# Optimization experiments

Measured on AMD Instinct MI355X. Metric: run time of the kernel, lower is better.

Reference implementation:

```python
import jax, jax.numpy as jnp
import numpy as np

TEMPERATURE = 34.0
PAD = 1  # kernel_size // 2

def setup_inputs() -> dict:
    key = jax.random.key(0)
    ks = jax.random.split(key, 5)
    B, C, H, W = 32, 256, 56, 56
    K, O, I, kh = 4, 256, 256, 3
    hidden = int(C * 0.25) + 1  # 65
    return {
        "x": jax.random.normal(ks[0], (B, C, H, W), jnp.float32),
        "fc1_w": jax.random.normal(ks[1], (hidden, C), jnp.float32) * (2.0 / C) ** 0.5,
        "fc2_w": jax.random.normal(ks[2], (K, hidden), jnp.float32) * (2.0 / hidden) ** 0.5,
        "fc2_b": jnp.zeros((K,), jnp.float32),
        "weight": jax.random.normal(ks[3], (K, O, I, kh, kh), jnp.float32) * (2.0 / (I * kh * kh)) ** 0.5,
        "bias": jnp.zeros((K, O), jnp.float32),
    }

def reference(x, fc1_w, fc2_w, fc2_b, weight, bias):
    # attention2d: global avg pool -> 1x1 conv (fc1) -> relu -> 1x1 conv (fc2) -> softmax(logits/T)
    pooled = x.mean(axis=(2, 3))                      # [B, C]
    h = jax.nn.relu(pooled @ fc1_w.T)                 # [B, hidden]
    logits = h @ fc2_w.T + fc2_b                      # [B, K]
    att = jax.nn.softmax(logits / TEMPERATURE, axis=1)
    # aggregate per-sample conv weights/bias over K kernel banks
    agg_w = jnp.einsum('bk,koihw->boihw', att, weight)  # [B, O, I, kh, kw]
    agg_b = att @ bias                                  # [B, O]
    # per-sample conv (torch emulates via groups=B): vmap over batch
    def conv_one(xi, wi):
        return jax.lax.conv_general_dilated(
            xi[None], wi, window_strides=(1, 1),
            padding=((PAD, PAD), (PAD, PAD)),
            dimension_numbers=('NCHW', 'OIHW', 'NCHW'))[0]
    out = jax.vmap(conv_one)(x, agg_w)                 # [B, O, H, W]
    return out + agg_b[:, :, None, None]
```

## Files before the change

### kernel.cpp

```cpp
#include <hip/hip_runtime.h>


typedef short bf16x8 __attribute__((ext_vector_type(8)));
typedef float f32x16 __attribute__((ext_vector_type(16)));

__device__ __forceinline__ unsigned short f2bf(float f) {
  unsigned int u = __float_as_uint(f);
  return (unsigned short)((u + 0x7FFFu + ((u >> 16) & 1u)) >> 16);
}
__device__ __forceinline__ float bf2f(unsigned short h) {
  return __uint_as_float(((unsigned int)h) << 16);
}

__device__ __forceinline__ int invswz(int S) {
  int b7 = (S >> 7) & 1;
  int b6 = ((S >> 6) & 1) ^ b7;
  int b5 = ((S >> 5) & 1) ^ b6;
  int b4 = ((S >> 4) & 1) ^ b5;
  return (S & ~0x70) | (b4 << 4) | (b5 << 5) | (b6 << 6);
}

typedef const __attribute__((address_space(1))) unsigned int* gas_t;
typedef __attribute__((address_space(3))) unsigned int* las_t;
__device__ __forceinline__ void dma16(const void* g, unsigned lds_addr) {
  __builtin_amdgcn_global_load_lds((gas_t)g, (las_t)(size_t)lds_addr, 16, 0, 0);
}

__global__ void xcast_k(const float* __restrict__ x, unsigned short* __restrict__ xb,
                        float* __restrict__ pooled) {
  __shared__ unsigned short tile[64 * 260];
  int b = blockIdx.y;
  int hw0 = blockIdx.x * 64;
  int t = threadIdx.x;
  int p = t & 15, g = t >> 4;
#pragma unroll
  for (int i = 0; i < 16; ++i) {
    int c = g + 16 * i;
    float4 v = *(const float4*)(x + ((size_t)(b * 256 + c)) * 3136 + hw0 + p * 4);
    tile[(p * 4 + 0) * 260 + c] = f2bf(v.x);
    tile[(p * 4 + 1) * 260 + c] = f2bf(v.y);
    tile[(p * 4 + 2) * 260 + c] = f2bf(v.z);
    tile[(p * 4 + 3) * 260 + c] = f2bf(v.w);
  }
  __syncthreads();
  int lane = t & 63, wq = t >> 6;
  int c4 = lane * 4;
#pragma unroll
  for (int it = 0; it < 16; ++it) {
    int hl = it * 4 + wq;
    ushort4 v = *(const ushort4*)&tile[hl * 260 + c4];
    *(ushort4*)&xb[((size_t)(b * 3136 + hw0 + hl)) * 256 + c4] = v;
  }
  float s = 0.f;
#pragma unroll 16
  for (int hl = 0; hl < 64; ++hl) s += bf2f(tile[hl * 260 + t]);
  atomicAdd(&pooled[b * 256 + t], s * (1.0f / 3136.0f));
}

__global__ void att_k(const float* __restrict__ pooled, const float* __restrict__ fc1,
                      const float* __restrict__ fc2w, const float* __restrict__ fc2b,
                      const float* __restrict__ bias, float* __restrict__ att,
                      float* __restrict__ aggb) {
  int b = blockIdx.x, t = threadIdx.x;
  __shared__ float p[256];
  __shared__ float h[65];
  __shared__ float a4[4];
  for (int i = t; i < 256; i += 64) p[i] = pooled[b * 256 + i];
  __syncthreads();
  for (int j = t; j < 65; j += 64) {
    float s = 0.f;
    for (int c = 0; c < 256; ++c) s += p[c] * fc1[j * 256 + c];
    h[j] = fmaxf(s, 0.f);
  }
  __syncthreads();
  if (t == 0) {
    float lg[4];
    for (int k = 0; k < 4; ++k) {
      float s = fc2b[k];
      for (int j = 0; j < 65; ++j) s += h[j] * fc2w[k * 65 + j];
      lg[k] = s * (1.0f / 34.0f);
    }
    float m = fmaxf(fmaxf(lg[0], lg[1]), fmaxf(lg[2], lg[3]));
    float e0 = expf(lg[0] - m), e1 = expf(lg[1] - m), e2 = expf(lg[2] - m), e3 = expf(lg[3] - m);
    float inv = 1.0f / (e0 + e1 + e2 + e3);
    a4[0] = e0 * inv; a4[1] = e1 * inv; a4[2] = e2 * inv; a4[3] = e3 * inv;
    for (int k = 0; k < 4; ++k) att[b * 4 + k] = a4[k];
  }
  __syncthreads();
  for (int o = t; o < 256; o += 64) {
    float s = 0.f;
    for (int k = 0; k < 4; ++k) s += a4[k] * bias[k * 256 + o];
    aggb[b * 256 + o] = s;
  }
}

__global__ void aggw_k(const float* __restrict__ weight, const float* __restrict__ att,
                       unsigned short* __restrict__ aggw) {
  __shared__ float wl[4 * 2304];
  int o = blockIdx.x, t = threadIdx.x;
  for (int k = 0; k < 4; ++k)
    for (int idx = t; idx < 2304; idx += 256)
      wl[k * 2304 + idx] = weight[((size_t)(k * 256 + o)) * 2304 + idx];
  __syncthreads();
  int ot = o >> 7, ol = o & 127, ic = t >> 4, il = t & 15;
  int b0 = blockIdx.y * 8;
  for (int b = b0; b < b0 + 8; ++b) {
    float a0 = att[b * 4 + 0], a1 = att[b * 4 + 1], a2 = att[b * 4 + 2], a3 = att[b * 4 + 3];
    size_t base = ((size_t)((b * 2 + ot) * 16 + ic)) * (9 * 2048) + ol * 16 + il;
#pragma unroll
    for (int r = 0; r < 9; ++r) {
      float s = a0 * wl[t * 9 + r] + a1 * wl[2304 + t * 9 + r] +
                a2 * wl[4608 + t * 9 + r] + a3 * wl[6912 + t * 9 + r];
      aggw[base + r * 2048] = f2bf(s);
    }
  }
}

#define XBUF 16384
#define AOFF 32768

__global__ __launch_bounds__(256, 2) void conv_k(const unsigned short* __restrict__ xb,
                                                 const unsigned short* __restrict__ aggw,
                                                 const float* __restrict__ aggb,
                                                 const float* __restrict__ zerobuf,
                                                 float* __restrict__ out) {
  extern __shared__ unsigned char lds[];
  const unsigned ldsbase = (unsigned)(size_t)&lds[0];
  const int t = threadIdx.x;
  const int wid = t >> 6, lane = t & 63, l31 = lane & 31, q = lane >> 5;
  const int wo = wid >> 1, wn = wid & 1;

  int id = blockIdx.x;
  int wgid = (id & 7) * 104 + (id >> 3);
  int bn = wgid % 13;
  int rest = wgid / 13;
  int b = rest >> 1, bo = rest & 1;

  const int o0 = bo * 128;
  const int n0 = bn * 256;
  const int h0 = n0 / 56;

  int bbase[4], nn[4], swz[4][3];
#pragma unroll
  for (int nf = 0; nf < 4; ++nf) {
    int n = n0 + wn * 128 + nf * 32 + l31;
    int h = n / 56, w = n - h * 56;
    nn[nf] = n;
    bbase[nf] = ((h - h0) * 64 + w) * 32 + q * 16;
#pragma unroll
    for (int dw = 0; dw < 3; ++dw) swz[nf][dw] = ((w + dw) & 7) << 4;
  }
  int abase[2];
#pragma unroll
  for (int mf = 0; mf < 2; ++mf) {
    int ol = wo * 64 + mf * 32 + l31;
    abase[mf] = AOFF + ((ol * 32 + q * 16) ^ ((ol & 7) << 4));
  }

  const char* xb_b = (const char*)xb + (size_t)b * 3136 * 512;
  const char* ag_c = (const char*)aggw + (size_t)rest * 589824;

  const char* xg[4];
#pragma unroll
  for (int j = 0; j < 4; ++j) {
    int S = (j * 256 + t) * 16;
    int L = invswz(S);
    int pos = L >> 5, sub = (L >> 4) & 1;
    int row = pos >> 6, col = pos & 63;
    int hg = h0 - 1 + row, wg = col - 1;
    bool valid = (col >= 1 && col <= 56 && hg >= 0 && hg < 56);
    xg[j] = valid ? (xb_b + (size_t)(hg * 56 + wg) * 512 + sub * 16) : (const char*)zerobuf;
  }
  const char* aL = ag_c + invswz(t * 16);

  f32x16 acc[2][4];
#pragma unroll
  for (int i = 0; i < 2; ++i)
#pragma unroll
    for (int j = 0; j < 4; ++j)
#pragma unroll
      for (int e = 0; e < 16; ++e) acc[i][j][e] = 0.f;

#pragma unroll
  for (int j = 0; j < 4; ++j) dma16(xg[j], ldsbase + j * 4096 + wid * 1024);
#pragma unroll
  for (int j = 0; j < 9; ++j) dma16(aL + j * 4096, ldsbase + AOFF + j * 4096 + wid * 1024);
  __syncthreads();

  int cur = 0;
  for (int ic = 0; ic < 16; ++ic) {
    const unsigned char* xlds = lds + cur * XBUF;
#pragma unroll
    for (int r = 0; r < 9; ++r) {
      const int dh = r / 3, dw = r % 3;
      bf16x8 a0 = *(const bf16x8*)(lds + abase[0] + r * 4096);
      bf16x8 a1 = *(const bf16x8*)(lds + abase[1] + r * 4096);
      bf16x8 b0 = *(const bf16x8*)(xlds + ((bbase[0] + dh * 2048 + dw * 32) ^ swz[0][dw]));
      bf16x8 b1 = *(const bf16x8*)(xlds + ((bbase[1] + dh * 2048 + dw * 32) ^ swz[1][dw]));
      bf16x8 b2 = *(const bf16x8*)(xlds + ((bbase[2] + dh * 2048 + dw * 32) ^ swz[2][dw]));
      bf16x8 b3 = *(const bf16x8*)(xlds + ((bbase[3] + dh * 2048 + dw * 32) ^ swz[3][dw]));
      __builtin_amdgcn_s_setprio(1);
      acc[0][0] = __builtin_amdgcn_mfma_f32_32x32x16_bf16(a0, b0, acc[0][0], 0, 0, 0);
      acc[0][1] = __builtin_amdgcn_mfma_f32_32x32x16_bf16(a0, b1, acc[0][1], 0, 0, 0);
      acc[0][2] = __builtin_amdgcn_mfma_f32_32x32x16_bf16(a0, b2, acc[0][2], 0, 0, 0);
      acc[0][3] = __builtin_amdgcn_mfma_f32_32x32x16_bf16(a0, b3, acc[0][3], 0, 0, 0);
      acc[1][0] = __builtin_amdgcn_mfma_f32_32x32x16_bf16(a1, b0, acc[1][0], 0, 0, 0);
      acc[1][1] = __builtin_amdgcn_mfma_f32_32x32x16_bf16(a1, b1, acc[1][1], 0, 0, 0);
      acc[1][2] = __builtin_amdgcn_mfma_f32_32x32x16_bf16(a1, b2, acc[1][2], 0, 0, 0);
      acc[1][3] = __builtin_amdgcn_mfma_f32_32x32x16_bf16(a1, b3, acc[1][3], 0, 0, 0);
      __builtin_amdgcn_s_setprio(0);
      if (r == 0 && ic + 1 < 16) {
#pragma unroll
        for (int j = 0; j < 4; ++j)
          dma16(xg[j] + (ic + 1) * 32, ldsbase + (cur ^ 1) * XBUF + j * 4096 + wid * 1024);
      }
    }
    __syncthreads();
    if (ic + 1 < 16) {
#pragma unroll
      for (int j = 0; j < 9; ++j)
        dma16(aL + (size_t)(ic + 1) * 36864 + j * 4096, ldsbase + AOFF + j * 4096 + wid * 1024);
      __syncthreads();
    }
    cur ^= 1;
  }

#pragma unroll
  for (int mf = 0; mf < 2; ++mf) {
#pragma unroll
    for (int reg = 0; reg < 16; ++reg) {
      int o = o0 + wo * 64 + mf * 32 + (reg & 3) + 8 * (reg >> 2) + 4 * q;
      float ab = aggb[b * 256 + o];
      float* op = out + ((size_t)(b * 256 + o)) * 3136;
#pragma unroll
      for (int nf = 0; nf < 4; ++nf) {
        if (nn[nf] < 3136) op[nn[nf]] = acc[mf][nf][reg] + ab;
      }
    }
  }
}

extern "C" void kernel_launch(void* const* d_in, const int* in_sizes, int n_in,
                              void* d_out, int out_size, void* d_ws, size_t ws_size,
                              hipStream_t stream) {
  const float* x      = (const float*)d_in[0];
  const float* fc1    = (const float*)d_in[1];
  const float* fc2w   = (const float*)d_in[2];
  const float* fc2b   = (const float*)d_in[3];
  const float* weight = (const float*)d_in[4];
  const float* bias   = (const float*)d_in[5];
  float* out = (float*)d_out;

  char* ws = (char*)d_ws;
  float* pooled         = (float*)(ws);
  float* att            = (float*)(ws + 32768);
  float* aggb           = (float*)(ws + 33280);
  unsigned short* aggw  = (unsigned short*)(ws + 66048);
  unsigned short* xb    = (unsigned short*)(ws + 66048 + 37748736);

  hipFuncSetAttribute(reinterpret_cast<const void*>(conv_k),
                      hipFuncAttributeMaxDynamicSharedMemorySize, 2 * XBUF + 36864);

  hipMemsetAsync(pooled, 0, 32768, stream);
  xcast_k<<<dim3(49, 32), 256, 0, stream>>>(x, xb, pooled);
  att_k<<<32, 64, 0, stream>>>(pooled, fc1, fc2w, fc2b, bias, att, aggb);
  hipMemsetAsync(pooled, 0, 1024, stream);
  aggw_k<<<dim3(256, 4), 256, 0, stream>>>(weight, att, aggw);
  conv_k<<<832, 256, 2 * XBUF + 36864, stream>>>(xb, aggw, aggb, (const float*)pooled, out);
}
```

Measured before the change: 232.7 us.

## Load aggregated weights directly into registers instead of staging through LDS

The conv kernel no longer stages per-sample weight tiles in LDS. Each wave now loads its A fragments for all nine taps straight from global memory into registers at the start of every channel chunk, and the x-tile prefetch moves to the same point. This drops the second barrier and cuts shared memory from about 69KB to 32KB per block, which may let more blocks fit per CU. The costs are higher register pressure (18 extra bf16x8 values per thread) and exposed global-load latency on the weight reads, since those are not double-buffered.

Result: slower. 257.1 us (+10.5%).

```diff
diff --git a/kernel.cpp b/kernel.cpp
--- a/kernel.cpp
+++ b/kernel.cpp
@@ -117,14 +117,13 @@
 }
 
 #define XBUF 16384
-#define AOFF 32768
 
 __global__ __launch_bounds__(256, 2) void conv_k(const unsigned short* __restrict__ xb,
                                                  const unsigned short* __restrict__ aggw,
                                                  const float* __restrict__ aggb,
                                                  const float* __restrict__ zerobuf,
                                                  float* __restrict__ out) {
-  extern __shared__ unsigned char lds[];
+  __shared__ __align__(16) unsigned char lds[2 * XBUF];
   const unsigned ldsbase = (unsigned)(size_t)&lds[0];
   const int t = threadIdx.x;
   const int wid = t >> 6, lane = t & 63, l31 = lane & 31, q = lane >> 5;
@@ -150,12 +149,9 @@
 #pragma unroll
     for (int dw = 0; dw < 3; ++dw) swz[nf][dw] = ((w + dw) & 7) << 4;
   }
-  int abase[2];
-#pragma unroll
-  for (int mf = 0; mf < 2; ++mf) {
-    int ol = wo * 64 + mf * 32 + l31;
-    abase[mf] = AOFF + ((ol * 32 + q * 16) ^ ((ol & 7) << 4));
-  }
+  int aoff[2];
+#pragma unroll
+  for (int mf = 0; mf < 2; ++mf) aoff[mf] = (wo * 64 + mf * 32 + l31) * 32 + q * 16;
 
   const char* xb_b = (const char*)xb + (size_t)b * 3136 * 512;
   const char* ag_c = (const char*)aggw + (size_t)rest * 589824;
@@ -171,7 +167,6 @@
     bool valid = (col >= 1 && col <= 56 && hg >= 0 && hg < 56);
     xg[j] = valid ? (xb_b + (size_t)(hg * 56 + wg) * 512 + sub * 16) : (const char*)zerobuf;
   }
-  const char* aL = ag_c + invswz(t * 16);
 
   f32x16 acc[2][4];
 #pragma unroll
@@ -183,45 +178,43 @@
 
 #pragma unroll
   for (int j = 0; j < 4; ++j) dma16(xg[j], ldsbase + j * 4096 + wid * 1024);
-#pragma unroll
-  for (int j = 0; j < 9; ++j) dma16(aL + j * 4096, ldsbase + AOFF + j * 4096 + wid * 1024);
   __syncthreads();
 
   int cur = 0;
   for (int ic = 0; ic < 16; ++ic) {
+    bf16x8 areg[2][9];
+    const char* agc = ag_c + (size_t)ic * 36864;
+#pragma unroll
+    for (int r = 0; r < 9; ++r) {
+      areg[0][r] = *(const bf16x8*)(agc + r * 4096 + aoff[0]);
+      areg[1][r] = *(const bf16x8*)(agc + r * 4096 + aoff[1]);
+    }
+    if (ic + 1 < 16) {
+#pragma unroll
+      for (int j = 0; j < 4; ++j)
+        dma16(xg[j] + (ic + 1) * 32, ldsbase + (cur ^ 1) * XBUF + j * 4096 + wid * 1024);
+    }
+    __builtin_amdgcn_sched_barrier(0);
     const unsigned char* xlds = lds + cur * XBUF;
 #pragma unroll
     for (int r = 0; r < 9; ++r) {
       const int dh = r / 3, dw = r % 3;
-      bf16x8 a0 = *(const bf16x8*)(lds + abase[0] + r * 4096);
-      bf16x8 a1 = *(const bf16x8*)(lds + abase[1] + r * 4096);
       bf16x8 b0 = *(const bf16x8*)(xlds + ((bbase[0] + dh * 2048 + dw * 32) ^ swz[0][dw]));
       bf16x8 b1 = *(const bf16x8*)(xlds + ((bbase[1] + dh * 2048 + dw * 32) ^ swz[1][dw]));
       bf16x8 b2 = *(const bf16x8*)(xlds + ((bbase[2] + dh * 2048 + dw * 32) ^ swz[2][dw]));
       bf16x8 b3 = *(const bf16x8*)(xlds + ((bbase[3] + dh * 2048 + dw * 32) ^ swz[3][dw]));
       __builtin_amdgcn_s_setprio(1);
-      acc[0][0] = __builtin_amdgcn_mfma_f32_32x32x16_bf16(a0, b0, acc[0][0], 0, 0, 0);
-      acc[0][1] = __builtin_amdgcn_mfma_f32_32x32x16_bf16(a0, b1, acc[0][1], 0, 0, 0);
-      acc[0][2] = __builtin_amdgcn_mfma_f32_32x32x16_bf16(a0, b2, acc[0][2], 0, 0, 0);
-      acc[0][3] = __builtin_amdgcn_mfma_f32_32x32x16_bf16(a0, b3, acc[0][3], 0, 0, 0);
-      acc[1][0] = __builtin_amdgcn_mfma_f32_32x32x16_bf16(a1, b0, acc[1][0], 0, 0, 0);
-      acc[1][1] = __builtin_amdgcn_mfma_f32_32x32x16_bf16(a1, b1, acc[1][1], 0, 0, 0);
-      acc[1][2] = __builtin_amdgcn_mfma_f32_32x32x16_bf16(a1, b2, acc[1][2], 0, 0, 0);
-      acc[1][3] = __builtin_amdgcn_mfma_f32_32x32x16_bf16(a1, b3, acc[1][3], 0, 0, 0);
+      acc[0][0] = __builtin_amdgcn_mfma_f32_32x32x16_bf16(areg[0][r], b0, acc[0][0], 0, 0, 0);
+      acc[0][1] = __builtin_amdgcn_mfma_f32_32x32x16_bf16(areg[0][r], b1, acc[0][1], 0, 0, 0);
+      acc[0][2] = __builtin_amdgcn_mfma_f32_32x32x16_bf16(areg[0][r], b2, acc[0][2], 0, 0, 0);
+      acc[0][3] = __builtin_amdgcn_mfma_f32_32x32x16_bf16(areg[0][r], b3, acc[0][3], 0, 0, 0);
+      acc[1][0] = __builtin_amdgcn_mfma_f32_32x32x16_bf16(areg[1][r], b0, acc[1][0], 0, 0, 0);
+      acc[1][1] = __builtin_amdgcn_mfma_f32_32x32x16_bf16(areg[1][r], b1, acc[1][1], 0, 0, 0);
+      acc[1][2] = __builtin_amdgcn_mfma_f32_32x32x16_bf16(areg[1][r], b2, acc[1][2], 0, 0, 0);
+      acc[1][3] = __builtin_amdgcn_mfma_f32_32x32x16_bf16(areg[1][r], b3, acc[1][3], 0, 0, 0);
       __builtin_amdgcn_s_setprio(0);
-      if (r == 0 && ic + 1 < 16) {
-#pragma unroll
-        for (int j = 0; j < 4; ++j)
-          dma16(xg[j] + (ic + 1) * 32, ldsbase + (cur ^ 1) * XBUF + j * 4096 + wid * 1024);
-      }
     }
     __syncthreads();
-    if (ic + 1 < 16) {
-#pragma unroll
-      for (int j = 0; j < 9; ++j)
-        dma16(aL + (size_t)(ic + 1) * 36864 + j * 4096, ldsbase + AOFF + j * 4096 + wid * 1024);
-      __syncthreads();
-    }
     cur ^= 1;
   }
 
@@ -258,13 +251,10 @@
   unsigned short* aggw  = (unsigned short*)(ws + 66048);
   unsigned short* xb    = (unsigned short*)(ws + 66048 + 37748736);
 
-  hipFuncSetAttribute(reinterpret_cast<const void*>(conv_k),
-                      hipFuncAttributeMaxDynamicSharedMemorySize, 2 * XBUF + 36864);
-
   hipMemsetAsync(pooled, 0, 32768, stream);
   xcast_k<<<dim3(49, 32), 256, 0, stream>>>(x, xb, pooled);
   att_k<<<32, 64, 0, stream>>>(pooled, fc1, fc2w, fc2b, bias, att, aggb);
   hipMemsetAsync(pooled, 0, 1024, stream);
   aggw_k<<<dim3(256, 4), 256, 0, stream>>>(weight, att, aggw);
-  conv_k<<<832, 256, 2 * XBUF + 36864, stream>>>(xb, aggw, aggb, (const float*)pooled, out);
-}
+  conv_k<<<832, 256, 0, stream>>>(xb, aggw, aggb, (const float*)pooled, out);
+}
```
